# Optimization experiments

Hardware: AMD Instinct MI355X
Metric: run time of the kernel (lower is better)

The kernel has to match this reference:

```python
import jax, jax.numpy as jnp
import numpy as np

BN_EPS = 1e-5


def setup_inputs() -> dict:
    key = jax.random.key(0)
    ks = jax.random.split(key, 8)
    N, H, OUT = 32 * 1024, 512, 32
    return {
        "x": jax.random.normal(ks[0], (N, 2), dtype=jnp.float32),
        "batch_size": 32,
        "Wq": jax.random.normal(ks[1], (2, H), dtype=jnp.float32) / np.sqrt(2.0),
        "Wk": jax.random.normal(ks[2], (2, H), dtype=jnp.float32) / np.sqrt(2.0),
        "Wv": jax.random.normal(ks[3], (2, H), dtype=jnp.float32) / np.sqrt(2.0),
        "bn_gamma": jnp.ones((H,), jnp.float32),
        "bn_beta": jnp.zeros((H,), jnp.float32),
        "bn_mean": jnp.zeros((H,), jnp.float32),
        "bn_var": jnp.ones((H,), jnp.float32),
        "prelu_a": jnp.full((1,), 0.25, jnp.float32),
        "W_out": jax.random.normal(ks[4], (H, OUT), dtype=jnp.float32) / np.sqrt(H),
        "b_out": jnp.zeros((OUT,), jnp.float32),
    }


def reference(x, batch_size, Wq, Wk, Wv, bn_gamma, bn_beta, bn_mean, bn_var,
              prelu_a, W_out, b_out):
    H = Wq.shape[1]
    # project tokens [N,2] -> [B,S,H]
    q = (x @ Wq).reshape(batch_size, -1, H)
    k = (x @ Wk).reshape(batch_size, -1, H)
    v = (x @ Wv).reshape(batch_size, -1, H)
    scale = 1.0 / jnp.sqrt(jnp.asarray(H, x.dtype))
    attn = jax.nn.softmax(jnp.einsum("bqh,bkh->bqk", q, k) * scale, axis=-1)
    out = jnp.einsum("bqk,bkh->bqh", attn, v).reshape(-1, H)  # [N,H]
    # BatchNorm1d (eval mode) + PReLU + Linear (dropout = identity in eval)
    out = (out - bn_mean) * (bn_gamma / jnp.sqrt(bn_var + BN_EPS)) + bn_beta
    out = jnp.where(out >= 0, out, prelu_a[0] * out)
    return out @ W_out + b_out
```

## Files before the change

kernel.cpp:

```cpp
#include <hip/hip_runtime.h>
#include <math.h>


#define H_DIM   512
#define OUT_DIM 32
#define S_LEN   1024
#define THREADS 256
#define NW 4

#define WS_WOUT 0
#define WS_ABC  32768
#define WS_M    40960
#define WS_AMAX 40976

#if __has_builtin(__builtin_amdgcn_exp2f)
#define EXP2(x) __builtin_amdgcn_exp2f(x)
#else
#define EXP2(x) exp2f(x)
#endif

typedef __attribute__((ext_vector_type(8))) short bf16x8;
typedef __attribute__((ext_vector_type(4))) float f32x4;

__device__ __forceinline__ unsigned int rne_bf16(float f) {
    unsigned int u = __float_as_uint(f);
    return (u + 0x7fffu + ((u >> 16) & 1u)) >> 16;
}
__device__ __forceinline__ unsigned int pack2bf16(float lo, float hi) {
    return rne_bf16(lo) | (rne_bf16(hi) << 16);
}

union frag_cast { unsigned int u[4]; int4 i4; bf16x8 v; };

__global__ __launch_bounds__(256)
void setup_kernel(const float* __restrict__ x,
                  const float* __restrict__ Wq, const float* __restrict__ Wk,
                  const float* __restrict__ Wv,
                  const float* __restrict__ gam, const float* __restrict__ bet,
                  const float* __restrict__ mean, const float* __restrict__ var,
                  const float* __restrict__ Wout,
                  unsigned char* __restrict__ ws)
{
    const int t = threadIdx.x;
    if (blockIdx.x < 16) {
        unsigned int* dst = (unsigned int*)(ws + WS_WOUT);
        #pragma unroll
        for (int k = 0; k < 2; ++k) {
            int pi = blockIdx.x * 512 + k * 256 + t;
            int d  = pi * 2;
            int fid = d >> 9;
            int l   = (d >> 3) & 63;
            int j   = d & 7;
            int nt  = fid >> 4;
            int s   = fid & 15;
            int h   = s * 32 + (l >> 4) * 8 + j;
            int o   = nt * 16 + (l & 15);
            float f0 = Wout[h * 32 + o];
            float f1 = Wout[(h + 1) * 32 + o];
            dst[pi] = pack2bf16(f0, f1);
        }
    } else {
        float4* abc = (float4*)(ws + WS_ABC);
        #pragma unroll
        for (int k = 0; k < 2; ++k) {
            int h = t + k * 256;
            float g = gam[h] * rsqrtf(var[h] + 1e-5f);
            abc[h] = make_float4(Wv[h] * g, Wv[H_DIM + h] * g,
                                 bet[h] - mean[h] * g, 0.f);
        }
        if (t < 64) {
            float m00 = 0.f, m01 = 0.f, m10 = 0.f, m11 = 0.f;
            #pragma unroll
            for (int k = 0; k < 8; ++k) {
                int h = t + k * 64;
                float a0 = Wq[h], a1 = Wq[H_DIM + h];
                float b0 = Wk[h], b1 = Wk[H_DIM + h];
                m00 = fmaf(a0, b0, m00); m01 = fmaf(a0, b1, m01);
                m10 = fmaf(a1, b0, m10); m11 = fmaf(a1, b1, m11);
            }
            #pragma unroll
            for (int off = 32; off >= 1; off >>= 1) {
                m00 += __shfl_xor(m00, off); m01 += __shfl_xor(m01, off);
                m10 += __shfl_xor(m10, off); m11 += __shfl_xor(m11, off);
            }
            if (t == 0) {
                const float scale = 0.044194173824159216f;
                float* m = (float*)(ws + WS_M);
                m[0] = m00 * scale; m[1] = m01 * scale;
                m[2] = m10 * scale; m[3] = m11 * scale;
            }
        }
        {
            int batch = t >> 3, sub = t & 7;
            const float4* xb = ((const float4*)x) + batch * 512;
            float a0 = 0.f, a1 = 0.f;
            for (int i = 0; i < 64; ++i) {
                float4 v = xb[sub + i * 8];
                a0 = fmaxf(a0, fmaxf(fabsf(v.x), fabsf(v.z)));
                a1 = fmaxf(a1, fmaxf(fabsf(v.y), fabsf(v.w)));
            }
            #pragma unroll
            for (int off = 4; off >= 1; off >>= 1) {
                a0 = fmaxf(a0, __shfl_xor(a0, off));
                a1 = fmaxf(a1, __shfl_xor(a1, off));
            }
            if (sub == 0)
                ((float2*)(ws + WS_AMAX))[batch] = make_float2(a0, a1);
        }
    }
}

__global__ __launch_bounds__(THREADS)
void fused_attn_kernel(const float* __restrict__ x,
                       const float* __restrict__ prelu_a,
                       const float* __restrict__ bout,
                       const unsigned char* __restrict__ ws,
                       float* __restrict__ out)
{
    __shared__ float2 xs[S_LEN];
    __shared__ float4 abcs[H_DIM];
    __shared__ float redl[NW][64], redw0[NW][64], redw1[NW][64];

    const int t    = threadIdx.x;
    const int lane = t & 63;
    const int q    = __builtin_amdgcn_readfirstlane(t >> 6);
    const int b    = blockIdx.x >> 4;
    const int tile = blockIdx.x & 15;

    const float4* xg = (const float4*)(x + (size_t)b * (S_LEN * 2));
    float4* xs4 = (float4*)xs;
    xs4[t]       = xg[t];
    xs4[t + 256] = xg[t + 256];
    const float4* abcg = (const float4*)(ws + WS_ABC);
    abcs[t]       = abcg[t];
    abcs[t + 256] = abcg[t + 256];

    const float* mp = (const float*)(ws + WS_M);
    const float m00 = mp[0], m01 = mp[1], m10 = mp[2], m11 = mp[3];
    const float2 am = ((const float2*)(ws + WS_AMAX))[b];
    __syncthreads();

    const float2 xt = xs[tile * 64 + lane];
    const float u0 = fmaf(xt.x, m00, xt.y * m10);
    const float u1 = fmaf(xt.x, m01, xt.y * m11);
    const float L2E = 1.4426950408889634f;
    const float bnd = fmaf(fabsf(u0), am.x, fabsf(u1) * am.y);
    const float u0L = u0 * L2E, u1L = u1 * L2E, nbL = -bnd * L2E;

    float l = 0.f, w0 = 0.f, w1 = 0.f;
    const float4* kv = ((const float4*)xs) + q * 128;
    #pragma unroll 4
    for (int i = 0; i < 128; ++i) {
        float4 k2 = kv[i];
        float e0 = EXP2(fmaf(u0L, k2.x, fmaf(u1L, k2.y, nbL)));
        float e1 = EXP2(fmaf(u0L, k2.z, fmaf(u1L, k2.w, nbL)));
        l += e0 + e1;
        w0 = fmaf(e0, k2.x, fmaf(e1, k2.z, w0));
        w1 = fmaf(e0, k2.y, fmaf(e1, k2.w, w1));
    }
    redl[q][lane] = l; redw0[q][lane] = w0; redw1[q][lane] = w1;
    __syncthreads();
    l  = redl[0][lane]  + redl[1][lane]  + redl[2][lane]  + redl[3][lane];
    w0 = redw0[0][lane] + redw0[1][lane] + redw0[2][lane] + redw0[3][lane];
    w1 = redw1[0][lane] + redw1[1][lane] + redw1[2][lane] + redw1[3][lane];
    const float inv = 1.0f / l;
    w0 *= inv; w1 *= inv;

    const int src = q * 16 + (lane & 15);
    const float w0t = __shfl(w0, src);
    const float w1t = __shfl(w1, src);

    const float ap = prelu_a[0];
    const int quad = lane >> 4;
    f32x4 acc0 = {0.f, 0.f, 0.f, 0.f};
    f32x4 acc1 = {0.f, 0.f, 0.f, 0.f};
    const int4* bsrc = (const int4*)(ws + WS_WOUT);

    for (int s = 0; s < 16; ++s) {
        frag_cast bf0, bf1;
        bf0.i4 = bsrc[s * 64 + lane];
        bf1.i4 = bsrc[(16 + s) * 64 + lane];
        const int hbase = s * 32 + quad * 8;
        frag_cast af;
        #pragma unroll
        for (int jj = 0; jj < 4; ++jj) {
            float4 c0 = abcs[hbase + jj * 2];
            float4 c1 = abcs[hbase + jj * 2 + 1];
            float z0 = fmaf(w0t, c0.x, fmaf(w1t, c0.y, c0.z));
            float z1 = fmaf(w0t, c1.x, fmaf(w1t, c1.y, c1.z));
            float p0 = fmaxf(z0, 0.f) + ap * fminf(z0, 0.f);
            float p1 = fmaxf(z1, 0.f) + ap * fminf(z1, 0.f);
            af.u[jj] = pack2bf16(p0, p1);
        }
        acc0 = __builtin_amdgcn_mfma_f32_16x16x32_bf16(af.v, bf0.v, acc0, 0, 0, 0);
        acc1 = __builtin_amdgcn_mfma_f32_16x16x32_bf16(af.v, bf1.v, acc1, 0, 0, 0);
    }

    const size_t base = (size_t)(b * S_LEN + tile * 64) * OUT_DIM;
    const int o0 = lane & 15;
    const float bo0 = bout[o0], bo1 = bout[16 + o0];
    #pragma unroll
    for (int r = 0; r < 4; ++r) {
        const int tt = q * 16 + quad * 4 + r;
        out[base + tt * 32 + o0]      = acc0[r] + bo0;
        out[base + tt * 32 + 16 + o0] = acc1[r] + bo1;
    }
}

extern "C" void kernel_launch(void* const* d_in, const int* in_sizes, int n_in,
                              void* d_out, int out_size, void* d_ws, size_t ws_size,
                              hipStream_t stream) {
    const float* x    = (const float*)d_in[0];
    const float* Wq   = (const float*)d_in[2];
    const float* Wk   = (const float*)d_in[3];
    const float* Wv   = (const float*)d_in[4];
    const float* gam  = (const float*)d_in[5];
    const float* bet  = (const float*)d_in[6];
    const float* mean = (const float*)d_in[7];
    const float* var  = (const float*)d_in[8];
    const float* pa   = (const float*)d_in[9];
    const float* Wout = (const float*)d_in[10];
    const float* bo   = (const float*)d_in[11];
    float* out = (float*)d_out;
    unsigned char* ws = (unsigned char*)d_ws;

    hipLaunchKernelGGL(setup_kernel, dim3(17), dim3(256), 0, stream,
                       x, Wq, Wk, Wv, gam, bet, mean, var, Wout, ws);

    const int N = in_sizes[0] / 2;
    const int blocks = N / 64;
    hipLaunchKernelGGL(fused_attn_kernel, dim3(blocks), dim3(THREADS), 0, stream,
                       x, pa, bo, ws, out);
}
```

Measured before the change: 97.35 us.

## Use 8 waves per block, splitting key loop and K-dimension of output GEMM

Doubles the block to 512 threads so each wave processes half as many keys in the softmax loop and half of the H dimension in the output MFMA loop. Partial GEMM results from the two K-halves are combined with shared-memory atomics, then written out as coalesced float4 stores with bias. The aim is more parallelism per block and better latency hiding. The cost is extra shared memory, LDS atomic traffic and an additional barrier.

```diff
diff --git a/kernel.cpp b/kernel.cpp
--- a/kernel.cpp
+++ b/kernel.cpp
@@ -5,8 +5,8 @@
 #define H_DIM   512
 #define OUT_DIM 32
 #define S_LEN   1024
-#define THREADS 256
-#define NW 4
+#define THREADS 512
+#define NW 8
 
 #define WS_WOUT 0
 #define WS_ABC  32768
@@ -110,7 +110,7 @@
     }
 }
 
-__global__ __launch_bounds__(THREADS)
+__global__ __launch_bounds__(THREADS, 4)
 void fused_attn_kernel(const float* __restrict__ x,
                        const float* __restrict__ prelu_a,
                        const float* __restrict__ bout,
@@ -120,6 +120,7 @@
     __shared__ float2 xs[S_LEN];
     __shared__ float4 abcs[H_DIM];
     __shared__ float redl[NW][64], redw0[NW][64], redw1[NW][64];
+    __shared__ float yout[64][33];
 
     const int t    = threadIdx.x;
     const int lane = t & 63;
@@ -129,11 +130,14 @@
 
     const float4* xg = (const float4*)(x + (size_t)b * (S_LEN * 2));
     float4* xs4 = (float4*)xs;
-    xs4[t]       = xg[t];
-    xs4[t + 256] = xg[t + 256];
+    xs4[t] = xg[t];
     const float4* abcg = (const float4*)(ws + WS_ABC);
-    abcs[t]       = abcg[t];
-    abcs[t + 256] = abcg[t + 256];
+    abcs[t] = abcg[t];
+    {
+        float* yflat = &yout[0][0];
+        #pragma unroll
+        for (int i = t; i < 64 * 33; i += THREADS) yflat[i] = 0.f;
+    }
 
     const float* mp = (const float*)(ws + WS_M);
     const float m00 = mp[0], m01 = mp[1], m10 = mp[2], m11 = mp[3];
@@ -148,9 +152,9 @@
     const float u0L = u0 * L2E, u1L = u1 * L2E, nbL = -bnd * L2E;
 
     float l = 0.f, w0 = 0.f, w1 = 0.f;
-    const float4* kv = ((const float4*)xs) + q * 128;
-    #pragma unroll 4
-    for (int i = 0; i < 128; ++i) {
+    const float4* kv = ((const float4*)xs) + q * 64;
+    #pragma unroll 8
+    for (int i = 0; i < 64; ++i) {
         float4 k2 = kv[i];
         float e0 = EXP2(fmaf(u0L, k2.x, fmaf(u1L, k2.y, nbL)));
         float e1 = EXP2(fmaf(u0L, k2.z, fmaf(u1L, k2.w, nbL)));
@@ -160,13 +164,18 @@
     }
     redl[q][lane] = l; redw0[q][lane] = w0; redw1[q][lane] = w1;
     __syncthreads();
-    l  = redl[0][lane]  + redl[1][lane]  + redl[2][lane]  + redl[3][lane];
-    w0 = redw0[0][lane] + redw0[1][lane] + redw0[2][lane] + redw0[3][lane];
-    w1 = redw1[0][lane] + redw1[1][lane] + redw1[2][lane] + redw1[3][lane];
+    l = 0.f; w0 = 0.f; w1 = 0.f;
+    #pragma unroll
+    for (int w = 0; w < NW; ++w) {
+        l  += redl[w][lane];
+        w0 += redw0[w][lane];
+        w1 += redw1[w][lane];
+    }
     const float inv = 1.0f / l;
     w0 *= inv; w1 *= inv;
 
-    const int src = q * 16 + (lane & 15);
+    const int tt = q & 3, kh = q >> 2;
+    const int src = tt * 16 + (lane & 15);
     const float w0t = __shfl(w0, src);
     const float w1t = __shfl(w1, src);
 
@@ -176,7 +185,9 @@
     f32x4 acc1 = {0.f, 0.f, 0.f, 0.f};
     const int4* bsrc = (const int4*)(ws + WS_WOUT);
 
-    for (int s = 0; s < 16; ++s) {
+    #pragma unroll 4
+    for (int si = 0; si < 8; ++si) {
+        const int s = kh * 8 + si;
         frag_cast bf0, bf1;
         bf0.i4 = bsrc[s * 64 + lane];
         bf1.i4 = bsrc[(16 + s) * 64 + lane];
@@ -196,14 +207,25 @@
         acc1 = __builtin_amdgcn_mfma_f32_16x16x32_bf16(af.v, bf1.v, acc1, 0, 0, 0);
     }
 
-    const size_t base = (size_t)(b * S_LEN + tile * 64) * OUT_DIM;
     const int o0 = lane & 15;
-    const float bo0 = bout[o0], bo1 = bout[16 + o0];
     #pragma unroll
     for (int r = 0; r < 4; ++r) {
-        const int tt = q * 16 + quad * 4 + r;
-        out[base + tt * 32 + o0]      = acc0[r] + bo0;
-        out[base + tt * 32 + 16 + o0] = acc1[r] + bo1;
+        const int tok = tt * 16 + quad * 4 + r;
+        atomicAdd(&yout[tok][o0],      acc0[r]);
+        atomicAdd(&yout[tok][16 + o0], acc1[r]);
+    }
+    __syncthreads();
+
+    {
+        const size_t base = (size_t)(b * S_LEN + tile * 64) * OUT_DIM;
+        const int tok = t >> 3, oq = t & 7;
+        const float4 b4 = ((const float4*)bout)[oq];
+        float4 v;
+        v.x = yout[tok][oq * 4 + 0] + b4.x;
+        v.y = yout[tok][oq * 4 + 1] + b4.y;
+        v.z = yout[tok][oq * 4 + 2] + b4.z;
+        v.w = yout[tok][oq * 4 + 3] + b4.w;
+        *(float4*)(out + base + (size_t)t * 4) = v;
     }
 }
 
```

Result: slower. 105.0 us (+7.9%).

## Shrink per-block token tile to 16 and split H across waves

Applied to the files above, without the earlier changes.

Each block now handles 16 query tokens instead of 64, giving 4x more blocks. Each wave's 64 lanes cover 16 tokens times 4 key slices, combined with xor shuffles and a shared-memory sum. The output projection is split across waves by H chunk, with partials combined through LDS atomics before a coalesced float2 store. This adds parallelism and occupancy (launch bounds 8) at the cost of reloading the batch's x and abc table per block and extra atomics.

```diff
diff --git a/kernel.cpp b/kernel.cpp
--- a/kernel.cpp
+++ b/kernel.cpp
@@ -5,6 +5,7 @@
 #define H_DIM   512
 #define OUT_DIM 32
 #define S_LEN   1024
+#define TOK     16
 #define THREADS 256
 #define NW 4
 
@@ -110,7 +111,7 @@
     }
 }
 
-__global__ __launch_bounds__(THREADS)
+__global__ __launch_bounds__(THREADS, 8)
 void fused_attn_kernel(const float* __restrict__ x,
                        const float* __restrict__ prelu_a,
                        const float* __restrict__ bout,
@@ -119,13 +120,14 @@
 {
     __shared__ float2 xs[S_LEN];
     __shared__ float4 abcs[H_DIM];
-    __shared__ float redl[NW][64], redw0[NW][64], redw1[NW][64];
+    __shared__ float redl[NW][16], redw0[NW][16], redw1[NW][16];
+    __shared__ float yout[TOK][33];
 
     const int t    = threadIdx.x;
     const int lane = t & 63;
     const int q    = __builtin_amdgcn_readfirstlane(t >> 6);
-    const int b    = blockIdx.x >> 4;
-    const int tile = blockIdx.x & 15;
+    const int b    = blockIdx.x >> 6;
+    const int tile = blockIdx.x & 63;
 
     const float4* xg = (const float4*)(x + (size_t)b * (S_LEN * 2));
     float4* xs4 = (float4*)xs;
@@ -134,13 +136,19 @@
     const float4* abcg = (const float4*)(ws + WS_ABC);
     abcs[t]       = abcg[t];
     abcs[t + 256] = abcg[t + 256];
+    {
+        float* yflat = &yout[0][0];
+        #pragma unroll
+        for (int i = t; i < TOK * 33; i += THREADS) yflat[i] = 0.f;
+    }
 
     const float* mp = (const float*)(ws + WS_M);
     const float m00 = mp[0], m01 = mp[1], m10 = mp[2], m11 = mp[3];
     const float2 am = ((const float2*)(ws + WS_AMAX))[b];
     __syncthreads();
 
-    const float2 xt = xs[tile * 64 + lane];
+    const int tok = lane & 15;
+    const float2 xt = xs[tile * TOK + tok];
     const float u0 = fmaf(xt.x, m00, xt.y * m10);
     const float u1 = fmaf(xt.x, m01, xt.y * m11);
     const float L2E = 1.4426950408889634f;
@@ -148,9 +156,10 @@
     const float u0L = u0 * L2E, u1L = u1 * L2E, nbL = -bnd * L2E;
 
     float l = 0.f, w0 = 0.f, w1 = 0.f;
-    const float4* kv = ((const float4*)xs) + q * 128;
-    #pragma unroll 4
-    for (int i = 0; i < 128; ++i) {
+    const int slice = q * 4 + (lane >> 4);
+    const float4* kv = ((const float4*)xs) + slice * 32;
+    #pragma unroll 8
+    for (int i = 0; i < 32; ++i) {
         float4 k2 = kv[i];
         float e0 = EXP2(fmaf(u0L, k2.x, fmaf(u1L, k2.y, nbL)));
         float e1 = EXP2(fmaf(u0L, k2.z, fmaf(u1L, k2.w, nbL)));
@@ -158,17 +167,20 @@
         w0 = fmaf(e0, k2.x, fmaf(e1, k2.z, w0));
         w1 = fmaf(e0, k2.y, fmaf(e1, k2.w, w1));
     }
-    redl[q][lane] = l; redw0[q][lane] = w0; redw1[q][lane] = w1;
+    l  += __shfl_xor(l, 16);  l  += __shfl_xor(l, 32);
+    w0 += __shfl_xor(w0, 16); w0 += __shfl_xor(w0, 32);
+    w1 += __shfl_xor(w1, 16); w1 += __shfl_xor(w1, 32);
+    if (lane < 16) { redl[q][lane] = l; redw0[q][lane] = w0; redw1[q][lane] = w1; }
     __syncthreads();
-    l  = redl[0][lane]  + redl[1][lane]  + redl[2][lane]  + redl[3][lane];
-    w0 = redw0[0][lane] + redw0[1][lane] + redw0[2][lane] + redw0[3][lane];
-    w1 = redw1[0][lane] + redw1[1][lane] + redw1[2][lane] + redw1[3][lane];
+    l = 0.f; w0 = 0.f; w1 = 0.f;
+    #pragma unroll
+    for (int w = 0; w < NW; ++w) {
+        l  += redl[w][tok];
+        w0 += redw0[w][tok];
+        w1 += redw1[w][tok];
+    }
     const float inv = 1.0f / l;
-    w0 *= inv; w1 *= inv;
-
-    const int src = q * 16 + (lane & 15);
-    const float w0t = __shfl(w0, src);
-    const float w1t = __shfl(w1, src);
+    const float w0t = w0 * inv, w1t = w1 * inv;
 
     const float ap = prelu_a[0];
     const int quad = lane >> 4;
@@ -176,7 +188,9 @@
     f32x4 acc1 = {0.f, 0.f, 0.f, 0.f};
     const int4* bsrc = (const int4*)(ws + WS_WOUT);
 
-    for (int s = 0; s < 16; ++s) {
+    #pragma unroll
+    for (int si = 0; si < 4; ++si) {
+        const int s = q * 4 + si;
         frag_cast bf0, bf1;
         bf0.i4 = bsrc[s * 64 + lane];
         bf1.i4 = bsrc[(16 + s) * 64 + lane];
@@ -196,14 +210,23 @@
         acc1 = __builtin_amdgcn_mfma_f32_16x16x32_bf16(af.v, bf1.v, acc1, 0, 0, 0);
     }
 
-    const size_t base = (size_t)(b * S_LEN + tile * 64) * OUT_DIM;
     const int o0 = lane & 15;
-    const float bo0 = bout[o0], bo1 = bout[16 + o0];
     #pragma unroll
     for (int r = 0; r < 4; ++r) {
-        const int tt = q * 16 + quad * 4 + r;
-        out[base + tt * 32 + o0]      = acc0[r] + bo0;
-        out[base + tt * 32 + 16 + o0] = acc1[r] + bo1;
+        const int tk = quad * 4 + r;
+        atomicAdd(&yout[tk][o0],      acc0[r]);
+        atomicAdd(&yout[tk][16 + o0], acc1[r]);
+    }
+    __syncthreads();
+
+    {
+        const size_t base = (size_t)(b * S_LEN + tile * TOK) * OUT_DIM;
+        const int tk = t >> 4, o = (t & 15) * 2;
+        const float2 b2 = ((const float2*)bout)[t & 15];
+        float2 v;
+        v.x = yout[tk][o]     + b2.x;
+        v.y = yout[tk][o + 1] + b2.y;
+        *(float2*)(out + base + (size_t)t * 2) = v;
     }
 }
 
@@ -228,7 +251,7 @@
                        x, Wq, Wk, Wv, gam, bet, mean, var, Wout, ws);
 
     const int N = in_sizes[0] / 2;
-    const int blocks = N / 64;
+    const int blocks = N / TOK;
     hipLaunchKernelGGL(fused_attn_kernel, dim3(blocks), dim3(THREADS), 0, stream,
                        x, pa, bo, ws, out);
 }
```

After: 114.5 us. +17.6%, slower.

## Fold setup kernel into attention kernel and drop softmax max-bound shift

Applied to the files above, without the earlier changes.

Removes the separate setup launch. Each block now builds its own BN/Wv coefficients, the Wq·Wk 2x2 matrix (block-wide reduction) and the bf16 MFMA fragments of W_out directly in LDS. It also drops the per-batch |x| max bound that was subtracted inside the exponent, so softmax is computed without a stability shift. This saves a kernel launch and the serial per-batch max scan, but every one of the 512 blocks redundantly reads and packs all of W_out. LDS use rises by 32KB per block, which may lower occupancy, and larger inputs could overflow exp2.

```diff
diff --git a/kernel.cpp b/kernel.cpp
--- a/kernel.cpp
+++ b/kernel.cpp
@@ -7,11 +7,6 @@
 #define S_LEN   1024
 #define THREADS 256
 #define NW 4
-
-#define WS_WOUT 0
-#define WS_ABC  32768
-#define WS_M    40960
-#define WS_AMAX 40976
 
 #if __has_builtin(__builtin_amdgcn_exp2f)
 #define EXP2(x) __builtin_amdgcn_exp2f(x)
@@ -32,128 +27,101 @@
 
 union frag_cast { unsigned int u[4]; int4 i4; bf16x8 v; };
 
-__global__ __launch_bounds__(256)
-void setup_kernel(const float* __restrict__ x,
-                  const float* __restrict__ Wq, const float* __restrict__ Wk,
-                  const float* __restrict__ Wv,
-                  const float* __restrict__ gam, const float* __restrict__ bet,
-                  const float* __restrict__ mean, const float* __restrict__ var,
-                  const float* __restrict__ Wout,
-                  unsigned char* __restrict__ ws)
-{
-    const int t = threadIdx.x;
-    if (blockIdx.x < 16) {
-        unsigned int* dst = (unsigned int*)(ws + WS_WOUT);
-        #pragma unroll
-        for (int k = 0; k < 2; ++k) {
-            int pi = blockIdx.x * 512 + k * 256 + t;
-            int d  = pi * 2;
-            int fid = d >> 9;
-            int l   = (d >> 3) & 63;
-            int j   = d & 7;
-            int nt  = fid >> 4;
-            int s   = fid & 15;
-            int h   = s * 32 + (l >> 4) * 8 + j;
-            int o   = nt * 16 + (l & 15);
-            float f0 = Wout[h * 32 + o];
-            float f1 = Wout[(h + 1) * 32 + o];
-            dst[pi] = pack2bf16(f0, f1);
-        }
-    } else {
-        float4* abc = (float4*)(ws + WS_ABC);
-        #pragma unroll
-        for (int k = 0; k < 2; ++k) {
-            int h = t + k * 256;
-            float g = gam[h] * rsqrtf(var[h] + 1e-5f);
-            abc[h] = make_float4(Wv[h] * g, Wv[H_DIM + h] * g,
-                                 bet[h] - mean[h] * g, 0.f);
-        }
-        if (t < 64) {
-            float m00 = 0.f, m01 = 0.f, m10 = 0.f, m11 = 0.f;
-            #pragma unroll
-            for (int k = 0; k < 8; ++k) {
-                int h = t + k * 64;
-                float a0 = Wq[h], a1 = Wq[H_DIM + h];
-                float b0 = Wk[h], b1 = Wk[H_DIM + h];
-                m00 = fmaf(a0, b0, m00); m01 = fmaf(a0, b1, m01);
-                m10 = fmaf(a1, b0, m10); m11 = fmaf(a1, b1, m11);
-            }
-            #pragma unroll
-            for (int off = 32; off >= 1; off >>= 1) {
-                m00 += __shfl_xor(m00, off); m01 += __shfl_xor(m01, off);
-                m10 += __shfl_xor(m10, off); m11 += __shfl_xor(m11, off);
-            }
-            if (t == 0) {
-                const float scale = 0.044194173824159216f;
-                float* m = (float*)(ws + WS_M);
-                m[0] = m00 * scale; m[1] = m01 * scale;
-                m[2] = m10 * scale; m[3] = m11 * scale;
-            }
-        }
-        {
-            int batch = t >> 3, sub = t & 7;
-            const float4* xb = ((const float4*)x) + batch * 512;
-            float a0 = 0.f, a1 = 0.f;
-            for (int i = 0; i < 64; ++i) {
-                float4 v = xb[sub + i * 8];
-                a0 = fmaxf(a0, fmaxf(fabsf(v.x), fabsf(v.z)));
-                a1 = fmaxf(a1, fmaxf(fabsf(v.y), fabsf(v.w)));
-            }
-            #pragma unroll
-            for (int off = 4; off >= 1; off >>= 1) {
-                a0 = fmaxf(a0, __shfl_xor(a0, off));
-                a1 = fmaxf(a1, __shfl_xor(a1, off));
-            }
-            if (sub == 0)
-                ((float2*)(ws + WS_AMAX))[batch] = make_float2(a0, a1);
-        }
-    }
-}
-
 __global__ __launch_bounds__(THREADS)
 void fused_attn_kernel(const float* __restrict__ x,
+                       const float* __restrict__ Wq,
+                       const float* __restrict__ Wk,
+                       const float* __restrict__ Wv,
+                       const float* __restrict__ bn_gamma,
+                       const float* __restrict__ bn_beta,
+                       const float* __restrict__ bn_mean,
+                       const float* __restrict__ bn_var,
                        const float* __restrict__ prelu_a,
+                       const float* __restrict__ Wout,
                        const float* __restrict__ bout,
-                       const unsigned char* __restrict__ ws,
                        float* __restrict__ out)
 {
     __shared__ float2 xs[S_LEN];
     __shared__ float4 abcs[H_DIM];
+    __shared__ unsigned int bfr[32 * 64 * 4];
     __shared__ float redl[NW][64], redw0[NW][64], redw1[NW][64];
+    __shared__ float mred[NW][4];
 
     const int t    = threadIdx.x;
     const int lane = t & 63;
     const int q    = __builtin_amdgcn_readfirstlane(t >> 6);
     const int b    = blockIdx.x >> 4;
     const int tile = blockIdx.x & 15;
+    const float scale = 0.044194173824159216f;
+    const float L2E   = 1.4426950408889634f;
 
     const float4* xg = (const float4*)(x + (size_t)b * (S_LEN * 2));
     float4* xs4 = (float4*)xs;
     xs4[t]       = xg[t];
     xs4[t + 256] = xg[t + 256];
-    const float4* abcg = (const float4*)(ws + WS_ABC);
-    abcs[t]       = abcg[t];
-    abcs[t + 256] = abcg[t + 256];
 
-    const float* mp = (const float*)(ws + WS_M);
-    const float m00 = mp[0], m01 = mp[1], m10 = mp[2], m11 = mp[3];
-    const float2 am = ((const float2*)(ws + WS_AMAX))[b];
+    #pragma unroll
+    for (int k = 0; k < 2; ++k) {
+        int h = t + k * 256;
+        float g = bn_gamma[h] * rsqrtf(bn_var[h] + 1e-5f);
+        abcs[h] = make_float4(Wv[h] * g, Wv[H_DIM + h] * g,
+                              bn_beta[h] - bn_mean[h] * g, 0.f);
+    }
+
+    {
+        float m00 = 0.f, m01 = 0.f, m10 = 0.f, m11 = 0.f;
+        #pragma unroll
+        for (int k = 0; k < 2; ++k) {
+            int h = t + k * 256;
+            float a0 = Wq[h], a1 = Wq[H_DIM + h];
+            float b0 = Wk[h], b1 = Wk[H_DIM + h];
+            m00 = fmaf(a0, b0, m00); m01 = fmaf(a0, b1, m01);
+            m10 = fmaf(a1, b0, m10); m11 = fmaf(a1, b1, m11);
+        }
+        #pragma unroll
+        for (int off = 32; off >= 1; off >>= 1) {
+            m00 += __shfl_xor(m00, off); m01 += __shfl_xor(m01, off);
+            m10 += __shfl_xor(m10, off); m11 += __shfl_xor(m11, off);
+        }
+        if (lane == 0) {
+            mred[q][0] = m00; mred[q][1] = m01;
+            mred[q][2] = m10; mred[q][3] = m11;
+        }
+    }
+
+    #pragma unroll
+    for (int k = 0; k < 32; ++k) {
+        int i    = k * 256 + t;
+        int c    = i & 15;
+        int jj   = (i >> 4) & 3;
+        int quad = (i >> 6) & 3;
+        int s    = (i >> 8) & 15;
+        int nt   = (i >> 12) & 1;
+        int h    = s * 32 + quad * 8 + 2 * jj;
+        int o    = nt * 16 + c;
+        float f0 = Wout[h * 32 + o];
+        float f1 = Wout[(h + 1) * 32 + o];
+        int F = (nt * 16 + s) * 256 + (quad * 16 + c) * 4 + jj;
+        bfr[F] = pack2bf16(f0, f1);
+    }
     __syncthreads();
 
+    float m00 = (mred[0][0] + mred[1][0] + mred[2][0] + mred[3][0]) * scale;
+    float m01 = (mred[0][1] + mred[1][1] + mred[2][1] + mred[3][1]) * scale;
+    float m10 = (mred[0][2] + mred[1][2] + mred[2][2] + mred[3][2]) * scale;
+    float m11 = (mred[0][3] + mred[1][3] + mred[2][3] + mred[3][3]) * scale;
+
     const float2 xt = xs[tile * 64 + lane];
-    const float u0 = fmaf(xt.x, m00, xt.y * m10);
-    const float u1 = fmaf(xt.x, m01, xt.y * m11);
-    const float L2E = 1.4426950408889634f;
-    const float bnd = fmaf(fabsf(u0), am.x, fabsf(u1) * am.y);
-    const float u0L = u0 * L2E, u1L = u1 * L2E, nbL = -bnd * L2E;
+    const float u0L = fmaf(xt.x, m00, xt.y * m10) * L2E;
+    const float u1L = fmaf(xt.x, m01, xt.y * m11) * L2E;
 
     float l = 0.f, w0 = 0.f, w1 = 0.f;
     const float4* kv = ((const float4*)xs) + q * 128;
     #pragma unroll 4
     for (int i = 0; i < 128; ++i) {
         float4 k2 = kv[i];
-        float e0 = EXP2(fmaf(u0L, k2.x, fmaf(u1L, k2.y, nbL)));
-        float e1 = EXP2(fmaf(u0L, k2.z, fmaf(u1L, k2.w, nbL)));
+        float e0 = EXP2(fmaf(u0L, k2.x, u1L * k2.y));
+        float e1 = EXP2(fmaf(u0L, k2.z, u1L * k2.w));
         l += e0 + e1;
         w0 = fmaf(e0, k2.x, fmaf(e1, k2.z, w0));
         w1 = fmaf(e0, k2.y, fmaf(e1, k2.w, w1));
@@ -174,7 +142,7 @@
     const int quad = lane >> 4;
     f32x4 acc0 = {0.f, 0.f, 0.f, 0.f};
     f32x4 acc1 = {0.f, 0.f, 0.f, 0.f};
-    const int4* bsrc = (const int4*)(ws + WS_WOUT);
+    const int4* bsrc = (const int4*)bfr;
 
     for (int s = 0; s < 16; ++s) {
         frag_cast bf0, bf1;
@@ -222,13 +190,9 @@
     const float* Wout = (const float*)d_in[10];
     const float* bo   = (const float*)d_in[11];
     float* out = (float*)d_out;
-    unsigned char* ws = (unsigned char*)d_ws;
-
-    hipLaunchKernelGGL(setup_kernel, dim3(17), dim3(256), 0, stream,
-                       x, Wq, Wk, Wv, gam, bet, mean, var, Wout, ws);
 
     const int N = in_sizes[0] / 2;
     const int blocks = N / 64;
     hipLaunchKernelGGL(fused_attn_kernel, dim3(blocks), dim3(THREADS), 0, stream,
-                       x, pa, bo, ws, out);
+                       x, Wq, Wk, Wv, gam, bet, mean, var, pa, Wout, bo, out);
 }
```

Result: faster. 93.30 us (-4.2%).
